# Optimization experiments

Measured on AMD Instinct MI355X. Metric: run time of the kernel, lower is better.

## Reference

```python
import jax, jax.numpy as jnp
import numpy as np

D = 256
H = 8
HD = D // H  # 32
EPS = 1e-5


def _ln(x, g, b):
    m = jnp.mean(x, axis=-1, keepdims=True)
    v = jnp.var(x, axis=-1, keepdims=True)
    return (x - m) * jax.lax.rsqrt(v + EPS) * g + b


def setup_inputs() -> dict:
    key = jax.random.key(0)
    ks = jax.random.split(key, 30)
    B = 131072
    s = 0.05

    def w(k, shape, scale=s):
        return jax.random.normal(k, shape, dtype=jnp.float32) * scale

    inp = {
        'f24': w(ks[0], (B, D), 1.0),
        'f77': w(ks[1], (B, D), 1.0),
        'fx': w(ks[2], (B, D), 1.0),
        'norm_g': jnp.ones((D,), jnp.float32),
        'norm_b': jnp.zeros((D,), jnp.float32),
        'Wq24': w(ks[3], (D, D)), 'bq24': w(ks[4], (D,)),
        'Wk24': w(ks[5], (D, D)), 'bk24': w(ks[6], (D,)),
        'Wv24': w(ks[7], (D, D)), 'bv24': w(ks[8], (D,)),
        'Wq77': w(ks[9], (D, D)), 'bq77': w(ks[10], (D,)),
        'Wk77': w(ks[11], (D, D)), 'bk77': w(ks[12], (D,)),
        'Wv77': w(ks[13], (D, D)), 'bv77': w(ks[14], (D,)),
        'Wqx': w(ks[15], (D, D)), 'bqx': w(ks[16], (D,)),
        'Wkx': w(ks[17], (D, D)), 'bkx': w(ks[18], (D,)),
        'Wvx': w(ks[19], (D, D)), 'bvx': w(ks[20], (D,)),
        'Wout': w(ks[21], (D, D)), 'bout': w(ks[22], (D,)),
        'radar_w': jnp.ones((3,), jnp.float32),
        'W1': w(ks[23], (D, 4 * D)), 'b1': w(ks[24], (4 * D,)),
        'W2': w(ks[25], (4 * D, D)), 'b2': w(ks[26], (D,)),
        'fnorm_g': jnp.ones((D,), jnp.float32),
        'fnorm_b': jnp.zeros((D,), jnp.float32),
    }
    return inp


def reference(f24, f77, fx, norm_g, norm_b,
              Wq24, bq24, Wk24, bk24, Wv24, bv24,
              Wq77, bq77, Wk77, bk77, Wv77, bv77,
              Wqx, bqx, Wkx, bkx, Wvx, bvx,
              Wout, bout, radar_w, W1, b1, W2, b2,
              fnorm_g, fnorm_b):
    B = f24.shape[0]
    residual = (f24 + f77 + fx) / 3.0
    n24 = _ln(f24, norm_g, norm_b)
    n77 = _ln(f77, norm_g, norm_b)
    nx = _ln(fx, norm_g, norm_b)

    def proj(x, W, b):
        return (x @ W + b).reshape(B, H, HD)

    q24 = proj(n24, Wq24, bq24); k24 = proj(n24, Wk24, bk24); v24 = proj(n24, Wv24, bv24)
    q77 = proj(n77, Wq77, bq77); k77 = proj(n77, Wk77, bk77); v77 = proj(n77, Wv77, bv77)
    qx = proj(nx, Wqx, bqx); kx = proj(nx, Wkx, bkx); vx = proj(nx, Wvx, bvx)

    scale = HD ** (-0.5)

    def att(q, ka, kb):  # [B,H,H] each
        a = jnp.einsum('bhd,bgd->bhg', q, ka) * scale
        b_ = jnp.einsum('bhd,bgd->bhg', q, kb) * scale
        # softmax across the two radar sources (stacked dim), NOT over keys
        return jax.nn.softmax(jnp.stack([a, b_], axis=1), axis=1)

    attn_24 = att(q24, k77, kx)
    attn_77 = att(q77, k24, kx)
    attn_x = att(qx, k24, k77)

    def mix(p, va, vb):  # [B,2,H,H] x [B,H,HD] -> [B, D]
        o = jnp.einsum('bhg,bgd->bhd', p[:, 0], va) + jnp.einsum('bhg,bgd->bhd', p[:, 1], vb)
        return o.reshape(B, D)

    out_24 = mix(attn_24, v77, vx)
    out_77 = mix(attn_77, v24, vx)
    out_x = mix(attn_x, v24, v77)

    rw = jax.nn.softmax(radar_w, axis=0)
    fused = rw[0] * out_24 + rw[1] * out_77 + rw[2] * out_x
    fused = fused @ Wout + bout
    fused = fused + residual
    ff = jax.nn.gelu(fused @ W1 + b1, approximate=False) @ W2 + b2  # dropout = eval identity
    output = _ln(fused + ff, fnorm_g, fnorm_b)
    return output, rw
```

## Files before the change

### kernel.cpp

```cpp
#include <hip/hip_runtime.h>

#define DEV __device__ __forceinline__

typedef float f4_t __attribute__((ext_vector_type(4)));
typedef short v8s  __attribute__((ext_vector_type(8)));

DEV float lo16(unsigned int w){ return __uint_as_float(w << 16); }
DEV float hi16(unsigned int w){ return __uint_as_float(w & 0xffff0000u); }
DEV unsigned short f2b(float f){
  unsigned int x = __float_as_uint(f);
  x += 0x7fffu + ((x >> 16) & 1u);
  return (unsigned short)(x >> 16);
}
DEV float geluf(float v){ return 0.5f * v * (1.0f + erff(v * 0.7071067811865475f)); }

DEV void gload_lds16(const unsigned short* g, unsigned short* l){
  __builtin_amdgcn_global_load_lds(
      (const __attribute__((address_space(1))) void*)g,
      (__attribute__((address_space(3))) void*)l, 16, 0, 0);
}

__global__ void k_prep(
    const float* Wq24, const float* Wk24, const float* Wv24,
    const float* Wq77, const float* Wk77, const float* Wv77,
    const float* Wqx,  const float* Wkx,  const float* Wvx,
    const float* bq24, const float* bk24, const float* bv24,
    const float* bq77, const float* bk77, const float* bv77,
    const float* bqx,  const float* bkx,  const float* bvx,
    const float* Wout, const float* W1,   const float* W2,
    const float* radar_w,
    unsigned short* wt_cat, unsigned short* wout_t,
    unsigned short* w1_t, unsigned short* w2_t,
    float* bias_cat, float* rwbuf, float* out_tail)
{
  long idx = (long)blockIdx.x * blockDim.x + threadIdx.x;
  if (idx < 589824){
    int s = (int)(idx / 196608);
    int r = (int)(idx % 196608);
    int ng = r >> 8, k = r & 255;
    int which = ng >> 8, n = ng & 255;
    const float* src;
    switch (s*3 + which){
      case 0: src = Wq24; break;  case 1: src = Wk24; break;  case 2: src = Wv24; break;
      case 3: src = Wq77; break;  case 4: src = Wk77; break;  case 5: src = Wv77; break;
      case 6: src = Wqx;  break;  case 7: src = Wkx;  break;  default: src = Wvx; break;
    }
    wt_cat[idx] = f2b(src[k*256 + n]);
    return;
  }
  idx -= 589824;
  if (idx < 65536){ int n = (int)(idx >> 8), k = (int)(idx & 255);
    wout_t[idx] = f2b(Wout[k*256 + n]); return; }
  idx -= 65536;
  if (idx < 262144){ int n = (int)(idx >> 8), k = (int)(idx & 255);
    w1_t[idx] = f2b(W1[k*1024 + n]); return; }
  idx -= 262144;
  if (idx < 262144){ int n = (int)(idx >> 10), k = (int)(idx & 1023);
    w2_t[idx] = f2b(W2[k*256 + n]); return; }
  idx -= 262144;
  if (idx < 2304){
    int s = (int)(idx / 768), j = (int)(idx % 768);
    int which = j >> 8, jj = j & 255;
    const float* src;
    switch (s*3 + which){
      case 0: src = bq24; break;  case 1: src = bk24; break;  case 2: src = bv24; break;
      case 3: src = bq77; break;  case 4: src = bk77; break;  case 5: src = bv77; break;
      case 6: src = bqx;  break;  case 7: src = bkx;  break;  default: src = bvx; break;
    }
    bias_cat[idx] = src[jj]; return;
  }
  idx -= 2304;
  if (idx < 3){
    float w0 = radar_w[0], w1v = radar_w[1], w2v = radar_w[2];
    float m = fmaxf(w0, fmaxf(w1v, w2v));
    float e0 = __expf(w0-m), e1 = __expf(w1v-m), e2 = __expf(w2v-m);
    float inv = 1.0f/(e0+e1+e2);
    float rw = (idx==0 ? e0 : (idx==1 ? e1 : e2)) * inv;
    rwbuf[idx] = rw; out_tail[idx] = rw;
  }
}

__global__ __launch_bounds__(256) void k_ln3(
    const float* __restrict__ f24, const float* __restrict__ f77, const float* __restrict__ fx,
    const float* __restrict__ gg, const float* __restrict__ bb,
    unsigned short* __restrict__ nbuf, float* __restrict__ resid, int rows)
{
  int wid = threadIdx.x >> 6, lane = threadIdx.x & 63;
  long row = (long)blockIdx.x*4 + wid;
  long base = row*256 + lane*4;
  f4_t x0 = *(const f4_t*)(f24 + base);
  f4_t x1 = *(const f4_t*)(f77 + base);
  f4_t x2 = *(const f4_t*)(fx  + base);
  float s[3], q[3];
  s[0]=x0.x+x0.y+x0.z+x0.w;
  s[1]=x1.x+x1.y+x1.z+x1.w;
  s[2]=x2.x+x2.y+x2.z+x2.w;
  q[0]=fmaf(x0.x,x0.x,fmaf(x0.y,x0.y,fmaf(x0.z,x0.z,x0.w*x0.w)));
  q[1]=fmaf(x1.x,x1.x,fmaf(x1.y,x1.y,fmaf(x1.z,x1.z,x1.w*x1.w)));
  q[2]=fmaf(x2.x,x2.x,fmaf(x2.y,x2.y,fmaf(x2.z,x2.z,x2.w*x2.w)));
  #pragma unroll
  for (int m=1;m<64;m<<=1){
    #pragma unroll
    for (int j=0;j<3;j++){ s[j]+=__shfl_xor(s[j],m); q[j]+=__shfl_xor(q[j],m); }
  }
  f4_t G  = *(const f4_t*)(gg + lane*4);
  f4_t Bv = *(const f4_t*)(bb + lane*4);
  long strm = (long)rows*256;
  {
    float mean = s[0]*(1.0f/256.0f);
    float rstd = rsqrtf(q[0]*(1.0f/256.0f) - mean*mean + 1e-5f);
    ushort4 o;
    o.x=f2b((x0.x-mean)*rstd*G.x+Bv.x); o.y=f2b((x0.y-mean)*rstd*G.y+Bv.y);
    o.z=f2b((x0.z-mean)*rstd*G.z+Bv.z); o.w=f2b((x0.w-mean)*rstd*G.w+Bv.w);
    *(ushort4*)(nbuf + base) = o;
  }
  {
    float mean = s[1]*(1.0f/256.0f);
    float rstd = rsqrtf(q[1]*(1.0f/256.0f) - mean*mean + 1e-5f);
    ushort4 o;
    o.x=f2b((x1.x-mean)*rstd*G.x+Bv.x); o.y=f2b((x1.y-mean)*rstd*G.y+Bv.y);
    o.z=f2b((x1.z-mean)*rstd*G.z+Bv.z); o.w=f2b((x1.w-mean)*rstd*G.w+Bv.w);
    *(ushort4*)(nbuf + strm + base) = o;
  }
  {
    float mean = s[2]*(1.0f/256.0f);
    float rstd = rsqrtf(q[2]*(1.0f/256.0f) - mean*mean + 1e-5f);
    ushort4 o;
    o.x=f2b((x2.x-mean)*rstd*G.x+Bv.x); o.y=f2b((x2.y-mean)*rstd*G.y+Bv.y);
    o.z=f2b((x2.z-mean)*rstd*G.z+Bv.z); o.w=f2b((x2.w-mean)*rstd*G.w+Bv.w);
    *(ushort4*)(nbuf + 2*strm + base) = o;
  }
  f4_t rs;
  rs.x=(x0.x+x1.x+x2.x)*(1.0f/3.0f);
  rs.y=(x0.y+x1.y+x2.y)*(1.0f/3.0f);
  rs.z=(x0.z+x1.z+x2.z)*(1.0f/3.0f);
  rs.w=(x0.w+x1.w+x2.w)*(1.0f/3.0f);
  *(f4_t*)(resid + base) = rs;
}

template<int EPI>
__global__ __launch_bounds__(256,2) void k_gemm256(
    const unsigned short* __restrict__ A, const unsigned short* __restrict__ Bt,
    const float* __restrict__ bias, const float* __restrict__ resid,
    float* __restrict__ outF, unsigned short* __restrict__ outH,
    long aBatch, long bBatch, long biasBatch, long oBatch, int ldOut)
{
  __shared__ __align__(16) unsigned short As[2][128][64];
  __shared__ __align__(16) unsigned short Bs[2][128][64];
  int tid = threadIdx.x, wid = tid >> 6, lane = tid & 63;
  long m0 = (long)blockIdx.x * 128;
  int  n0 = blockIdx.y * 128;
  const unsigned short* Ab = A  + (long)blockIdx.z*aBatch + m0*256;
  const unsigned short* Bb = Bt + (long)blockIdx.z*bBatch + (long)n0*256;

  auto stage = [&](int bi, int k0){
    #pragma unroll
    for (int i=0;i<4;i++){
      int c = (wid*4+i)*64 + lane;
      int r = c >> 3, col = c & 7;
      gload_lds16(Ab + (long)r*256 + k0 + col*8, &As[bi][0][0] + (long)(wid*4+i)*512);
      gload_lds16(Bb + (long)r*256 + k0 + col*8, &Bs[bi][0][0] + (long)(wid*4+i)*512);
    }
  };

  f4_t acc[4][4] = {};
  int wm = (wid >> 1)*64, wn = (wid & 1)*64;
  int lr = lane & 15, lk = lane >> 4;

  stage(0, 0);
  for (int it=0; it<4; ++it){
    __syncthreads();
    if (it < 3) stage((it+1)&1, (it+1)*64);
    int cur = it & 1;
    #pragma unroll
    for (int ks=0; ks<2; ++ks){
      v8s af[4], bfv[4];
      #pragma unroll
      for (int f=0; f<4; f++){
        af[f]  = *(const v8s*)&As[cur][wm + f*16 + lr][ks*32 + lk*8];
        bfv[f] = *(const v8s*)&Bs[cur][wn + f*16 + lr][ks*32 + lk*8];
      }
      #pragma unroll
      for (int fm=0; fm<4; fm++)
        #pragma unroll
        for (int fn=0; fn<4; fn++)
          acc[fm][fn] = __builtin_amdgcn_mfma_f32_16x16x32_bf16(af[fm], bfv[fn], acc[fm][fn], 0,0,0);
    }
  }

  long zo = (long)blockIdx.z * oBatch;
  const float* bp = bias + (long)blockIdx.z * biasBatch;
  #pragma unroll
  for (int fm=0; fm<4; fm++){
    #pragma unroll
    for (int fn=0; fn<4; fn++){
      long gm = m0 + wm + fm*16 + lk*4;
      int  gn = n0 + wn + fn*16 + lr;
      float bv = bp[gn];
      #pragma unroll
      for (int r=0; r<4; r++){
        float v = acc[fm][fn][r] + bv;
        long o = zo + (gm + r)*(long)ldOut + gn;
        if (EPI == 0){
          outH[o] = f2b(v);
        } else if (EPI == 1){
          v += resid[o];
          outF[o] = v; outH[o] = f2b(v);
        } else {
          outH[o] = f2b(geluf(v));
        }
      }
    }
  }
}

__global__ __launch_bounds__(512,4) void k_attn(
    const unsigned short* __restrict__ qkv, const float* __restrict__ rwb,
    unsigned short* __restrict__ outA, int rows)
{
  __shared__ __align__(16) unsigned short L[8][72][40];
  int tid = threadIdx.x, wid = tid >> 6, lane = tid & 63;
  long brow0 = (long)blockIdx.x * 8;
  for (int c = tid; c < 2304; c += 512){
    int row = c / 288, rem = c % 288;
    int s = rem / 96, cc = rem % 96;
    int vi = cc >> 2, ch = cc & 3;
    const uint4* src = (const uint4*)(qkv + ((long)s*rows + brow0 + row)*768 + cc*8);
    *(uint4*)&L[row][s*24 + vi][ch*8] = *src;
  }
  __syncthreads();

  int h = lane >> 3, g = lane & 7;
  const unsigned short* R = &L[wid][0][0];
  float comb[32];
  #pragma unroll
  for (int i=0;i<32;i++) comb[i] = 0.0f;
  float rw0 = rwb[0], rw1 = rwb[1], rw2 = rwb[2];

  #pragma unroll
  for (int att=0; att<3; ++att){
    int qs  = att;
    int as_ = (att==0) ? 1 : 0;
    int bs_ = (att==2) ? 1 : 2;
    float rwv = (att==0) ? rw0 : ((att==1) ? rw1 : rw2);
    const unsigned short* qp  = R + (qs *24      + h)*40;
    const unsigned short* kap = R + (as_*24 + 8  + g)*40;
    const unsigned short* kbp = R + (bs_*24 + 8  + g)*40;
    float a = 0.0f, b = 0.0f;
    #pragma unroll
    for (int j=0;j<4;j++){
      uint4 qc  = *(const uint4*)(qp  + j*8);
      uint4 kac = *(const uint4*)(kap + j*8);
      uint4 kbc = *(const uint4*)(kbp + j*8);
      #define DOT2(QW,KA,KB) { float q0=lo16(QW), q1=hi16(QW); \
        a=fmaf(q0,lo16(KA),a); a=fmaf(q1,hi16(KA),a); \
        b=fmaf(q0,lo16(KB),b); b=fmaf(q1,hi16(KB),b); }
      DOT2(qc.x, kac.x, kbc.x) DOT2(qc.y, kac.y, kbc.y)
      DOT2(qc.z, kac.z, kbc.z) DOT2(qc.w, kac.w, kbc.w)
      #undef DOT2
    }
    float d  = (b - a) * 0.17677669529663689f;
    float p0 = 1.0f / (1.0f + __expf(d));
    float p1 = 1.0f - p0;
    float w0 = rwv * p0, w1 = rwv * p1;
    const unsigned short* vap = R + (as_*24 + 16 + g)*40;
    const unsigned short* vbp = R + (bs_*24 + 16 + g)*40;
    #pragma unroll
    for (int j=0;j<4;j++){
      uint4 va = *(const uint4*)(vap + j*8);
      uint4 vb = *(const uint4*)(vbp + j*8);
      #define MIX2(VA,VB,C0,C1) { \
        C0 = fmaf(w0, lo16(VA), fmaf(w1, lo16(VB), C0)); \
        C1 = fmaf(w0, hi16(VA), fmaf(w1, hi16(VB), C1)); }
      MIX2(va.x, vb.x, comb[j*8+0], comb[j*8+1])
      MIX2(va.y, vb.y, comb[j*8+2], comb[j*8+3])
      MIX2(va.z, vb.z, comb[j*8+4], comb[j*8+5])
      MIX2(va.w, vb.w, comb[j*8+6], comb[j*8+7])
      #undef MIX2
    }
  }

  float t16[16];
  { bool up = (lane & 4) != 0;
    #pragma unroll
    for (int i=0;i<16;i++){
      float send = up ? comb[i] : comb[16+i];
      float keep = up ? comb[16+i] : comb[i];
      t16[i] = keep + __shfl_xor(send, 4);
    } }
  float t8[8];
  { bool up = (lane & 2) != 0;
    #pragma unroll
    for (int i=0;i<8;i++){
      float send = up ? t16[i] : t16[8+i];
      float keep = up ? t16[8+i] : t16[i];
      t8[i] = keep + __shfl_xor(send, 2);
    } }
  float t4[4];
  { bool up = (lane & 1) != 0;
    #pragma unroll
    for (int i=0;i<4;i++){
      float send = up ? t8[i] : t8[4+i];
      float keep = up ? t8[4+i] : t8[i];
      t4[i] = keep + __shfl_xor(send, 1);
    } }

  long orow = brow0 + wid;
  ushort4 o4;
  o4.x = f2b(t4[0]); o4.y = f2b(t4[1]); o4.z = f2b(t4[2]); o4.w = f2b(t4[3]);
  *(ushort4*)(outA + orow*256 + lane*4) = o4;
}

__global__ __launch_bounds__(512,4) void k_ff2ln(
    const unsigned short* __restrict__ A, const unsigned short* __restrict__ Bt,
    const float* __restrict__ b2, const float* __restrict__ fusedF,
    const float* __restrict__ fg, const float* __restrict__ fb,
    float* __restrict__ dout)
{
  __shared__ __align__(16) union {
    struct { unsigned short As[2][64][64]; unsigned short Bs[2][256][64]; } st;
    float rowbuf[64][260];
  } u;
  int tid = threadIdx.x, wid = tid >> 6, lane = tid & 63;
  long m0 = (long)blockIdx.x * 64;
  const unsigned short* Ab = A + m0*1024;

  auto stage = [&](int bi, int k0){
    { int c = wid*64 + lane; int r = c >> 3, col = c & 7;
      gload_lds16(Ab + (long)r*1024 + k0 + col*8, &u.st.As[bi][0][0] + (long)wid*512); }
    #pragma unroll
    for (int i=0;i<4;i++){
      int j = wid*4 + i; int c = j*64 + lane; int r = c >> 3, col = c & 7;
      gload_lds16(Bt + (long)r*1024 + k0 + col*8, &u.st.Bs[bi][0][0] + (long)j*512);
    }
  };

  f4_t acc[2][4] = {};
  int wm = (wid >> 2)*32, wn = (wid & 3)*64;
  int lr = lane & 15, lk = lane >> 4;

  stage(0, 0);
  for (int it=0; it<16; ++it){
    __syncthreads();
    if (it < 15) stage((it+1)&1, (it+1)*64);
    int cur = it & 1;
    #pragma unroll
    for (int ks=0; ks<2; ++ks){
      v8s af[2], bfv[4];
      #pragma unroll
      for (int f=0; f<2; f++)
        af[f]  = *(const v8s*)&u.st.As[cur][wm + f*16 + lr][ks*32 + lk*8];
      #pragma unroll
      for (int f=0; f<4; f++)
        bfv[f] = *(const v8s*)&u.st.Bs[cur][wn + f*16 + lr][ks*32 + lk*8];
      #pragma unroll
      for (int fm=0; fm<2; fm++)
        #pragma unroll
        for (int fn=0; fn<4; fn++)
          acc[fm][fn] = __builtin_amdgcn_mfma_f32_16x16x32_bf16(af[fm], bfv[fn], acc[fm][fn], 0,0,0);
    }
  }
  __syncthreads();

  #pragma unroll
  for (int fm=0; fm<2; fm++){
    #pragma unroll
    for (int fn=0; fn<4; fn++){
      int rl = wm + fm*16 + lk*4;
      int cl = wn + fn*16 + lr;
      float bv = b2[cl];
      #pragma unroll
      for (int r=0; r<4; r++){
        float v = acc[fm][fn][r] + bv + fusedF[(m0 + rl + r)*256 + cl];
        u.rowbuf[rl + r][cl] = v;
      }
    }
  }
  __syncthreads();

  f4_t G  = *(const f4_t*)(fg + lane*4);
  f4_t Bv = *(const f4_t*)(fb + lane*4);
  #pragma unroll
  for (int rr=0; rr<8; ++rr){
    int row = wid*8 + rr;
    f4_t x = *(const f4_t*)&u.rowbuf[row][lane*4];
    float s = x.x + x.y + x.z + x.w;
    float q = fmaf(x.x,x.x, fmaf(x.y,x.y, fmaf(x.z,x.z, x.w*x.w)));
    #pragma unroll
    for (int m=1;m<64;m<<=1){ s += __shfl_xor(s,m); q += __shfl_xor(q,m); }
    float mean = s*(1.0f/256.0f);
    float rstd = rsqrtf(q*(1.0f/256.0f) - mean*mean + 1e-5f);
    f4_t o;
    o.x = (x.x-mean)*rstd*G.x + Bv.x;
    o.y = (x.y-mean)*rstd*G.y + Bv.y;
    o.z = (x.z-mean)*rstd*G.z + Bv.z;
    o.w = (x.w-mean)*rstd*G.w + Bv.w;
    *(f4_t*)(dout + (m0 + row)*256 + lane*4) = o;
  }
}

extern "C" void kernel_launch(void* const* d_in, const int* in_sizes, int n_in,
                              void* d_out, int out_size, void* d_ws, size_t ws_size,
                              hipStream_t stream)
{
  const float* f24    = (const float*)d_in[0];
  const float* f77    = (const float*)d_in[1];
  const float* fx     = (const float*)d_in[2];
  const float* norm_g = (const float*)d_in[3];
  const float* norm_b = (const float*)d_in[4];
  const float* Wq24 = (const float*)d_in[5];  const float* bq24 = (const float*)d_in[6];
  const float* Wk24 = (const float*)d_in[7];  const float* bk24 = (const float*)d_in[8];
  const float* Wv24 = (const float*)d_in[9];  const float* bv24 = (const float*)d_in[10];
  const float* Wq77 = (const float*)d_in[11]; const float* bq77 = (const float*)d_in[12];
  const float* Wk77 = (const float*)d_in[13]; const float* bk77 = (const float*)d_in[14];
  const float* Wv77 = (const float*)d_in[15]; const float* bv77 = (const float*)d_in[16];
  const float* Wqx  = (const float*)d_in[17]; const float* bqx  = (const float*)d_in[18];
  const float* Wkx  = (const float*)d_in[19]; const float* bkx  = (const float*)d_in[20];
  const float* Wvx  = (const float*)d_in[21]; const float* bvx  = (const float*)d_in[22];
  const float* Wout = (const float*)d_in[23]; const float* bout = (const float*)d_in[24];
  const float* radar_w = (const float*)d_in[25];
  const float* W1 = (const float*)d_in[26];   const float* b1 = (const float*)d_in[27];
  const float* W2 = (const float*)d_in[28];   const float* b2 = (const float*)d_in[29];
  const float* fnorm_g = (const float*)d_in[30];
  const float* fnorm_b = (const float*)d_in[31];

  const long Brows = (long)in_sizes[0] / 256;
  float* dout = (float*)d_out;
  char* ws = (char*)d_ws;

  size_t off = 0;
  auto A_ = [&](size_t b){ size_t o = off; off = (off + b + 255) & ~(size_t)255; return o; };
  size_t oWT = A_((size_t)3*768*256*2);
  size_t oWO = A_((size_t)65536*2);
  size_t oW1 = A_((size_t)262144*2);
  size_t oW2 = A_((size_t)262144*2);
  size_t oBC = A_((size_t)2304*4);
  size_t oRW = A_(256);
  size_t fixedEnd = off;

  unsigned short* WT_CAT = (unsigned short*)(ws + oWT);
  unsigned short* WOUT_T = (unsigned short*)(ws + oWO);
  unsigned short* W1_T   = (unsigned short*)(ws + oW1);
  unsigned short* W2_T   = (unsigned short*)(ws + oW2);
  float*          BIASC  = (float*)(ws + oBC);
  float*          RW     = (float*)(ws + oRW);

  const size_t PER_ROW = 7168;
  if (ws_size <= fixedEnd + 512) return;
  long maxR = (long)((ws_size - fixedEnd - 256) / PER_ROW);
  maxR &= ~127L;
  if (maxR < 128) return;
  long Rc = maxR < 16384 ? maxR : 16384;
  if (Rc > Brows) Rc = Brows;
  long nch = (Brows + Rc - 1) / Rc;
  Rc = ((Brows + nch - 1) / nch + 127) & ~127L;

  size_t chunkBase = (fixedEnd + 255) & ~(size_t)255;
  char* NB_B = ws + chunkBase;
  char* RS_B = NB_B + (size_t)1536*Rc;
  char* QK_B = RS_B + (size_t)1024*Rc;

  {
    long total = 589824 + 65536 + 262144 + 262144 + 2304 + 3;
    int blocks = (int)((total + 255) / 256);
    k_prep<<<blocks, 256, 0, stream>>>(
        Wq24, Wk24, Wv24, Wq77, Wk77, Wv77, Wqx, Wkx, Wvx,
        bq24, bk24, bv24, bq77, bk77, bv77, bqx, bkx, bvx,
        Wout, W1, W2, radar_w,
        WT_CAT, WOUT_T, W1_T, W2_T, BIASC, RW, dout + (size_t)Brows*256);
  }

  for (long row0 = 0; row0 < Brows; row0 += Rc){
    long rows = Brows - row0 < Rc ? Brows - row0 : Rc;
    unsigned short* NBUF   = (unsigned short*)NB_B;
    float*          RESID  = (float*)RS_B;
    unsigned short* QKV    = (unsigned short*)QK_B;
    unsigned short* ATTN   = (unsigned short*)NB_B;
    float*          FUSEDF = (float*)(NB_B + (size_t)rows*256*2);
    unsigned short* FUSEDH = (unsigned short*)QK_B;
    unsigned short* HBUF   = (unsigned short*)(QK_B + (size_t)rows*256*2);

    k_ln3<<<(int)(rows/4), 256, 0, stream>>>(
        f24 + row0*256, f77 + row0*256, fx + row0*256,
        norm_g, norm_b, NBUF, RESID, (int)rows);

    k_gemm256<0><<<dim3((int)(rows/128), 6, 3), 256, 0, stream>>>(
        NBUF, WT_CAT, BIASC, nullptr, nullptr, QKV,
        rows*256L, 768L*256, 768L, rows*768L, 768);

    k_attn<<<(int)(rows/8), 512, 0, stream>>>(QKV, RW, ATTN, (int)rows);

    k_gemm256<1><<<dim3((int)(rows/128), 2, 1), 256, 0, stream>>>(
        ATTN, WOUT_T, bout, RESID, FUSEDF, FUSEDH, 0, 0, 0, 0, 256);

    k_gemm256<2><<<dim3((int)(rows/128), 8, 1), 256, 0, stream>>>(
        FUSEDH, W1_T, b1, nullptr, nullptr, HBUF, 0, 0, 0, 0, 1024);

    k_ff2ln<<<(int)(rows/64), 512, 0, stream>>>(
        HBUF, W2_T, b2, FUSEDF, fnorm_g, fnorm_b, dout + row0*256);
  }
}
```

Measured before the change: 1.509 ms.

## Make GEMMs persistent with cross-tile prefetch, LDS swizzle and vectorized epilogues

The 256-K GEMM kernel becomes persistent: a grid of at most 512 blocks strides over tiles, and the next tile's K-chunk is prefetched while the current one is computed, with explicit vmcnt waits and raw barriers replacing __syncthreads. Both GEMM kernels now XOR-swizzle LDS columns to reduce bank conflicts. MFMA operands are swapped so each lane holds four consecutive columns, which allows vectorized bias, residual and output stores. The fp32 fused copy is dropped, and the FF2 residual is read from the bf16 buffer instead, which saves memory traffic but lowers residual precision.

```diff
diff --git a/kernel.cpp b/kernel.cpp
--- a/kernel.cpp
+++ b/kernel.cpp
@@ -7,6 +7,7 @@
 
 DEV float lo16(unsigned int w){ return __uint_as_float(w << 16); }
 DEV float hi16(unsigned int w){ return __uint_as_float(w & 0xffff0000u); }
+DEV float b2f(unsigned short u){ return __uint_as_float((unsigned)u << 16); }
 DEV unsigned short f2b(float f){
   unsigned int x = __float_as_uint(f);
   x += 0x7fffu + ((x >> 16) & 1u);
@@ -19,6 +20,11 @@
       (const __attribute__((address_space(1))) void*)g,
       (__attribute__((address_space(3))) void*)l, 16, 0, 0);
 }
+
+#define WAITV(n) asm volatile("s_waitcnt vmcnt(" #n ")" ::: "memory")
+#define SBAR()  do{ __builtin_amdgcn_sched_barrier(0); \
+                    asm volatile("s_barrier" ::: "memory"); \
+                    __builtin_amdgcn_sched_barrier(0); }while(0)
 
 __global__ void k_prep(
     const float* Wq24, const float* Wk24, const float* Wv24,
@@ -142,75 +148,96 @@
 __global__ __launch_bounds__(256,2) void k_gemm256(
     const unsigned short* __restrict__ A, const unsigned short* __restrict__ Bt,
     const float* __restrict__ bias, const float* __restrict__ resid,
-    float* __restrict__ outF, unsigned short* __restrict__ outH,
-    long aBatch, long bBatch, long biasBatch, long oBatch, int ldOut)
+    unsigned short* __restrict__ outH,
+    long aBatch, long bBatch, long biasBatch, long oBatch, int ldOut,
+    int tM, int tN, int tZ)
 {
   __shared__ __align__(16) unsigned short As[2][128][64];
   __shared__ __align__(16) unsigned short Bs[2][128][64];
   int tid = threadIdx.x, wid = tid >> 6, lane = tid & 63;
-  long m0 = (long)blockIdx.x * 128;
-  int  n0 = blockIdx.y * 128;
-  const unsigned short* Ab = A  + (long)blockIdx.z*aBatch + m0*256;
-  const unsigned short* Bb = Bt + (long)blockIdx.z*bBatch + (long)n0*256;
-
-  auto stage = [&](int bi, int k0){
+  int wm = (wid >> 1)*64, wn = (wid & 1)*64;
+  int lr = lane & 15, lk = lane >> 4;
+
+  int total = tM*tN*tZ;
+  int nT = (total - (int)blockIdx.x + (int)gridDim.x - 1) / (int)gridDim.x;
+  if (nT <= 0) return;
+  int G = nT*4;
+
+  auto tileOf = [&](int j, long& m0, int& n0, int& z){
+    int T = (int)blockIdx.x + j*(int)gridDim.x;
+    int mt = T % tM; int rest = T / tM;
+    int nt = rest % tN; z = rest / tN;
+    m0 = (long)mt*128; n0 = nt*128;
+  };
+
+  auto stage = [&](int g){
+    long m0; int n0, z;
+    tileOf(g >> 2, m0, n0, z);
+    int k0 = (g & 3)*64, bi = g & 1;
+    const unsigned short* Ab = A  + (long)z*aBatch + m0*256;
+    const unsigned short* Bb = Bt + (long)z*bBatch + (long)n0*256;
     #pragma unroll
     for (int i=0;i<4;i++){
       int c = (wid*4+i)*64 + lane;
-      int r = c >> 3, col = c & 7;
-      gload_lds16(Ab + (long)r*256 + k0 + col*8, &As[bi][0][0] + (long)(wid*4+i)*512);
-      gload_lds16(Bb + (long)r*256 + k0 + col*8, &Bs[bi][0][0] + (long)(wid*4+i)*512);
+      int r = c >> 3, sl = (c & 7) ^ (r & 7);
+      gload_lds16(Ab + (long)r*256 + k0 + sl*8, &As[bi][0][0] + (long)(wid*4+i)*512);
+      gload_lds16(Bb + (long)r*256 + k0 + sl*8, &Bs[bi][0][0] + (long)(wid*4+i)*512);
     }
   };
 
+  const f4_t fz = {0.f,0.f,0.f,0.f};
   f4_t acc[4][4] = {};
-  int wm = (wid >> 1)*64, wn = (wid & 1)*64;
-  int lr = lane & 15, lk = lane >> 4;
-
-  stage(0, 0);
-  for (int it=0; it<4; ++it){
-    __syncthreads();
-    if (it < 3) stage((it+1)&1, (it+1)*64);
-    int cur = it & 1;
+
+  stage(0);
+  for (int g=0; g<G; ++g){
+    if (g+1 < G){ stage(g+1); WAITV(8); }
+    else        { WAITV(0); }
+    SBAR();
+    int cur = g & 1;
     #pragma unroll
     for (int ks=0; ks<2; ++ks){
       v8s af[4], bfv[4];
       #pragma unroll
       for (int f=0; f<4; f++){
-        af[f]  = *(const v8s*)&As[cur][wm + f*16 + lr][ks*32 + lk*8];
-        bfv[f] = *(const v8s*)&Bs[cur][wn + f*16 + lr][ks*32 + lk*8];
+        int prA = wm + f*16 + lr;
+        int prB = wn + f*16 + lr;
+        int js  = ks*4 + lk;
+        af[f]  = *(const v8s*)&As[cur][prA][(js ^ (prA & 7))*8];
+        bfv[f] = *(const v8s*)&Bs[cur][prB][(js ^ (prB & 7))*8];
       }
       #pragma unroll
       for (int fm=0; fm<4; fm++)
         #pragma unroll
         for (int fn=0; fn<4; fn++)
-          acc[fm][fn] = __builtin_amdgcn_mfma_f32_16x16x32_bf16(af[fm], bfv[fn], acc[fm][fn], 0,0,0);
-    }
-  }
-
-  long zo = (long)blockIdx.z * oBatch;
-  const float* bp = bias + (long)blockIdx.z * biasBatch;
-  #pragma unroll
-  for (int fm=0; fm<4; fm++){
-    #pragma unroll
-    for (int fn=0; fn<4; fn++){
-      long gm = m0 + wm + fm*16 + lk*4;
-      int  gn = n0 + wn + fn*16 + lr;
-      float bv = bp[gn];
+          acc[fm][fn] = __builtin_amdgcn_mfma_f32_16x16x32_bf16(bfv[fn], af[fm], acc[fm][fn], 0,0,0);
+    }
+    if ((g & 3) == 3){
+      long m0; int n0, z;
+      tileOf(g >> 2, m0, n0, z);
+      long zo = (long)z*oBatch;
+      const float* bp = bias + (long)z*biasBatch;
       #pragma unroll
-      for (int r=0; r<4; r++){
-        float v = acc[fm][fn][r] + bv;
-        long o = zo + (gm + r)*(long)ldOut + gn;
-        if (EPI == 0){
-          outH[o] = f2b(v);
-        } else if (EPI == 1){
-          v += resid[o];
-          outF[o] = v; outH[o] = f2b(v);
-        } else {
-          outH[o] = f2b(geluf(v));
+      for (int fm=0; fm<4; fm++){
+        long gm = m0 + wm + fm*16 + lr;
+        long rowo = zo + gm*(long)ldOut;
+        #pragma unroll
+        for (int fn=0; fn<4; fn++){
+          int gn = n0 + wn + fn*16 + lk*4;
+          f4_t bv = *(const f4_t*)(bp + gn);
+          f4_t v = acc[fm][fn];
+          v.x += bv.x; v.y += bv.y; v.z += bv.z; v.w += bv.w;
+          if (EPI == 1){
+            f4_t rv = *(const f4_t*)(resid + rowo + gn);
+            v.x += rv.x; v.y += rv.y; v.z += rv.z; v.w += rv.w;
+          }
+          if (EPI == 2){ v.x=geluf(v.x); v.y=geluf(v.y); v.z=geluf(v.z); v.w=geluf(v.w); }
+          ushort4 o; o.x=f2b(v.x); o.y=f2b(v.y); o.z=f2b(v.z); o.w=f2b(v.w);
+          *(ushort4*)(outH + rowo + gn) = o;
+          acc[fm][fn] = fz;
         }
       }
     }
+    SBAR();
   }
 }
 
@@ -313,25 +340,26 @@
 
 __global__ __launch_bounds__(512,4) void k_ff2ln(
     const unsigned short* __restrict__ A, const unsigned short* __restrict__ Bt,
-    const float* __restrict__ b2, const float* __restrict__ fusedF,
+    const float* __restrict__ b2, const unsigned short* __restrict__ fusedH,
     const float* __restrict__ fg, const float* __restrict__ fb,
     float* __restrict__ dout)
 {
   __shared__ __align__(16) union {
     struct { unsigned short As[2][64][64]; unsigned short Bs[2][256][64]; } st;
-    float rowbuf[64][260];
+    float rowbuf[64][264];
   } u;
   int tid = threadIdx.x, wid = tid >> 6, lane = tid & 63;
   long m0 = (long)blockIdx.x * 64;
   const unsigned short* Ab = A + m0*1024;
 
-  auto stage = [&](int bi, int k0){
-    { int c = wid*64 + lane; int r = c >> 3, col = c & 7;
-      gload_lds16(Ab + (long)r*1024 + k0 + col*8, &u.st.As[bi][0][0] + (long)wid*512); }
+  auto stage = [&](int it){
+    int k0 = (it)*64, bi = it & 1;
+    { int c = wid*64 + lane; int r = c >> 3, sl = (c & 7) ^ (r & 7);
+      gload_lds16(Ab + (long)r*1024 + k0 + sl*8, &u.st.As[bi][0][0] + (long)wid*512); }
     #pragma unroll
     for (int i=0;i<4;i++){
-      int j = wid*4 + i; int c = j*64 + lane; int r = c >> 3, col = c & 7;
-      gload_lds16(Bt + (long)r*1024 + k0 + col*8, &u.st.Bs[bi][0][0] + (long)j*512);
+      int j = wid*4 + i; int c = j*64 + lane; int r = c >> 3, sl = (c & 7) ^ (r & 7);
+      gload_lds16(Bt + (long)r*1024 + k0 + sl*8, &u.st.Bs[bi][0][0] + (long)j*512);
     }
   };
 
@@ -339,41 +367,48 @@
   int wm = (wid >> 2)*32, wn = (wid & 3)*64;
   int lr = lane & 15, lk = lane >> 4;
 
-  stage(0, 0);
+  stage(0);
   for (int it=0; it<16; ++it){
-    __syncthreads();
-    if (it < 15) stage((it+1)&1, (it+1)*64);
+    if (it+1 < 16){ stage(it+1); WAITV(5); }
+    else          { WAITV(0); }
+    SBAR();
     int cur = it & 1;
     #pragma unroll
     for (int ks=0; ks<2; ++ks){
       v8s af[2], bfv[4];
       #pragma unroll
-      for (int f=0; f<2; f++)
-        af[f]  = *(const v8s*)&u.st.As[cur][wm + f*16 + lr][ks*32 + lk*8];
+      for (int f=0; f<2; f++){
+        int pr = wm + f*16 + lr;
+        af[f]  = *(const v8s*)&u.st.As[cur][pr][((ks*4+lk) ^ (pr & 7))*8];
+      }
       #pragma unroll
-      for (int f=0; f<4; f++)
-        bfv[f] = *(const v8s*)&u.st.Bs[cur][wn + f*16 + lr][ks*32 + lk*8];
+      for (int f=0; f<4; f++){
+        int pr = wn + f*16 + lr;
+        bfv[f] = *(const v8s*)&u.st.Bs[cur][pr][((ks*4+lk) ^ (pr & 7))*8];
+      }
       #pragma unroll
       for (int fm=0; fm<2; fm++)
         #pragma unroll
         for (int fn=0; fn<4; fn++)
-          acc[fm][fn] = __builtin_amdgcn_mfma_f32_16x16x32_bf16(af[fm], bfv[fn], acc[fm][fn], 0,0,0);
-    }
-  }
-  __syncthreads();
+          acc[fm][fn] = __builtin_amdgcn_mfma_f32_16x16x32_bf16(bfv[fn], af[fm], acc[fm][fn], 0,0,0);
+    }
+    SBAR();
+  }
 
   #pragma unroll
   for (int fm=0; fm<2; fm++){
+    int rl = wm + fm*16 + lr;
     #pragma unroll
     for (int fn=0; fn<4; fn++){
-      int rl = wm + fm*16 + lk*4;
-      int cl = wn + fn*16 + lr;
-      float bv = b2[cl];
-      #pragma unroll
-      for (int r=0; r<4; r++){
-        float v = acc[fm][fn][r] + bv + fusedF[(m0 + rl + r)*256 + cl];
-        u.rowbuf[rl + r][cl] = v;
-      }
+      int cl = wn + fn*16 + lk*4;
+      f4_t bv = *(const f4_t*)(b2 + cl);
+      ushort4 fh = *(const ushort4*)(fusedH + (m0 + rl)*256 + cl);
+      f4_t v = acc[fm][fn];
+      v.x += bv.x + b2f(fh.x);
+      v.y += bv.y + b2f(fh.y);
+      v.z += bv.z + b2f(fh.z);
+      v.w += bv.w + b2f(fh.w);
+      *(f4_t*)&u.rowbuf[rl][cl] = v;
     }
   }
   __syncthreads();
@@ -476,27 +511,33 @@
     float*          RESID  = (float*)RS_B;
     unsigned short* QKV    = (unsigned short*)QK_B;
     unsigned short* ATTN   = (unsigned short*)NB_B;
-    float*          FUSEDF = (float*)(NB_B + (size_t)rows*256*2);
     unsigned short* FUSEDH = (unsigned short*)QK_B;
     unsigned short* HBUF   = (unsigned short*)(QK_B + (size_t)rows*256*2);
+
+    int tM = (int)(rows/128);
 
     k_ln3<<<(int)(rows/4), 256, 0, stream>>>(
         f24 + row0*256, f77 + row0*256, fx + row0*256,
         norm_g, norm_b, NBUF, RESID, (int)rows);
 
-    k_gemm256<0><<<dim3((int)(rows/128), 6, 3), 256, 0, stream>>>(
-        NBUF, WT_CAT, BIASC, nullptr, nullptr, QKV,
-        rows*256L, 768L*256, 768L, rows*768L, 768);
+    { int tiles = tM*6*3; int grid = tiles < 512 ? tiles : 512;
+      k_gemm256<0><<<grid, 256, 0, stream>>>(
+          NBUF, WT_CAT, BIASC, nullptr, QKV,
+          rows*256L, 768L*256, 768L, rows*768L, 768, tM, 6, 3); }
 
     k_attn<<<(int)(rows/8), 512, 0, stream>>>(QKV, RW, ATTN, (int)rows);
 
-    k_gemm256<1><<<dim3((int)(rows/128), 2, 1), 256, 0, stream>>>(
-        ATTN, WOUT_T, bout, RESID, FUSEDF, FUSEDH, 0, 0, 0, 0, 256);
-
-    k_gemm256<2><<<dim3((int)(rows/128), 8, 1), 256, 0, stream>>>(
-        FUSEDH, W1_T, b1, nullptr, nullptr, HBUF, 0, 0, 0, 0, 1024);
+    { int tiles = tM*2; int grid = tiles < 512 ? tiles : 512;
+      k_gemm256<1><<<grid, 256, 0, stream>>>(
+          ATTN, WOUT_T, bout, RESID, FUSEDH,
+          0, 0, 0, 0, 256, tM, 2, 1); }
+
+    { int tiles = tM*8; int grid = tiles < 512 ? tiles : 512;
+      k_gemm256<2><<<grid, 256, 0, stream>>>(
+          FUSEDH, W1_T, b1, nullptr, HBUF,
+          0, 0, 0, 0, 1024, tM, 8, 1); }
 
     k_ff2ln<<<(int)(rows/64), 512, 0, stream>>>(
-        HBUF, W2_T, b2, FUSEDF, fnorm_g, fnorm_b, dout + row0*256);
-  }
-}
+        HBUF, W2_T, b2, FUSEDH, fnorm_g, fnorm_b, dout + row0*256);
+  }
+}
```

Measured after the change: 1.445 ms. 1.04x faster.
